# Performance work log

Hardware: AMD Instinct MI355X
Metric: run time of the kernel (lower is better)

## Reference

```python
import jax, jax.numpy as jnp
import numpy as np

N = 50000
E = 800000
IN_FT = 256
OUT_FT = 64


def setup_inputs() -> dict:
    key = jax.random.key(0)
    k_seq, k_w, k_src, k_dst, k_val = jax.random.split(key, 5)
    seq = jax.random.normal(k_seq, (N, IN_FT), dtype=jnp.float32)
    # xavier_uniform_ for fc.weight [out_ft, in_ft]
    limit = float(np.sqrt(6.0 / (IN_FT + OUT_FT)))
    W = jax.random.uniform(k_w, (OUT_FT, IN_FT), minval=-limit, maxval=limit, dtype=jnp.float32)
    bias = jnp.zeros((OUT_FT,), dtype=jnp.float32)          # bias.data.fill_(0.0)
    alpha = jnp.full((1,), 0.25, dtype=jnp.float32)         # PReLU default init
    edge_src = jax.random.randint(k_src, (E,), 0, N, dtype=jnp.int32)
    edge_dst = jax.random.randint(k_dst, (E,), 0, N, dtype=jnp.int32)
    edge_val = jax.random.uniform(k_val, (E,), dtype=jnp.float32)
    return {"seq": seq, "W": W, "bias": bias, "alpha": alpha,
            "edge_src": edge_src, "edge_dst": edge_dst, "edge_val": edge_val}


def reference(seq, W, bias, alpha, edge_src, edge_dst, edge_val):
    # fc(seq): [N, in_ft] @ [in_ft, out_ft] -> [N, out_ft]
    fts = jnp.einsum('ni,oi->no', seq, W)
    # spmm(adj, fts): gather source features, scale by edge value, scatter-add to dst
    msgs = fts[edge_src] * edge_val[:, None]                # [E, out_ft]
    out = jax.ops.segment_sum(msgs, edge_dst, num_segments=seq.shape[0])
    out = out + bias
    # PReLU with scalar (single-channel) alpha
    return jnp.where(out >= 0, out, alpha * out)
```

## Files before the change

### kernel.cpp

```cpp
#include <hip/hip_runtime.h>
#include <hip/hip_fp16.h>

#define IN_FT 256
#define OUT_FT 64

constexpr int BIN_LOG   = 6;
constexpr int BIN_NODES = 1 << BIN_LOG;
constexpr int MAX_NBIN  = 1024;
constexpr int BIN_CAP   = 1536;
constexpr int SC_BLOCKS = 256;

constexpr float FXS  = 2097152.0f;
constexpr float IFXS = 1.0f / 2097152.0f;

typedef _Float16 half8 __attribute__((ext_vector_type(8)));
typedef float    f32x4 __attribute__((ext_vector_type(4)));

__global__ __launch_bounds__(256) void wconv_kernel(
    const float* __restrict__ W, half8* __restrict__ Wh)
{
    int item = (int)blockIdx.x * 256 + (int)threadIdx.x;
    int l  = item & 63;
    int kc = (item >> 6) & 7;
    int nt = item >> 9;
    int m  = l & 15;
    int q  = l >> 4;
    const float* wp = W + (size_t)(nt * 16 + m) * IN_FT + kc * 32 + q * 8;
    float4 w0 = *(const float4*)wp;
    float4 w1 = *(const float4*)(wp + 4);
    half8 hh;
    hh[0] = (_Float16)w0.x; hh[1] = (_Float16)w0.y;
    hh[2] = (_Float16)w0.z; hh[3] = (_Float16)w0.w;
    hh[4] = (_Float16)w1.x; hh[5] = (_Float16)w1.y;
    hh[6] = (_Float16)w1.z; hh[7] = (_Float16)w1.w;
    Wh[item] = hh;
}

__global__ __launch_bounds__(256, 4) void fused_gemm_scatter(
    const float* __restrict__ seq, const half8* __restrict__ WhG,
    __half* __restrict__ fts, int N, int G,
    const int* __restrict__ src, const int* __restrict__ dst,
    const float* __restrict__ val, int* __restrict__ binCursor,
    int2* __restrict__ binned, int E, int NBIN)
{
    __shared__ alignas(16) char smem[32768];
    const int t = (int)threadIdx.x;

    if ((int)blockIdx.x < SC_BLOCKS) {
        int* h    = (int*)smem;
        int* base = h + MAX_NBIN;
        const int sb = (int)blockIdx.x;
        for (int i = t; i < NBIN; i += 256) h[i] = 0;
        __syncthreads();
        const int chunk = (E + SC_BLOCKS - 1) / SC_BLOCKS;
        const int s0 = sb * chunk;
        const int e0 = min(s0 + chunk, E);
#pragma unroll 4
        for (int i = s0 + t; i < e0; i += 256) atomicAdd(&h[dst[i] >> BIN_LOG], 1);
        __syncthreads();
        for (int i = t; i < NBIN; i += 256) {
            int c = h[i];
            base[i] = c ? atomicAdd(&binCursor[i], c) : 0;
            h[i] = 0;
        }
        __syncthreads();
#pragma unroll 4
        for (int i = s0 + t; i < e0; i += 256) {
            int d = dst[i];
            int b = d >> BIN_LOG;
            int pos = base[b] + atomicAdd(&h[b], 1);
            if (pos < BIN_CAP) {
                int2 pr;
                pr.x = src[i] | ((d & (BIN_NODES - 1)) << 16);
                pr.y = __float_as_int(val[i] * FXS);
                binned[(size_t)b * BIN_CAP + pos] = pr;
            }
        }
        return;
    }

    const int wave = t >> 6;
    const int l    = t & 63;
    int nodeBase = ((int)blockIdx.x - SC_BLOCKS) * 64 + wave * 16;
    const bool active = (nodeBase < N);
    if (nodeBase > N - 16) nodeBase = N - 16;
    const int m = l & 15;
    const int q = l >> 4;
    const float* ap = seq + (size_t)(nodeBase + m) * IN_FT + q * 8;

    float4 A[16];
#pragma unroll
    for (int kc = 0; kc < 8; ++kc) {
        A[2 * kc]     = *(const float4*)(ap + kc * 32);
        A[2 * kc + 1] = *(const float4*)(ap + kc * 32 + 4);
    }
    {
        const int4* wg  = (const int4*)WhG;
        int4*       bsw = (int4*)smem;
#pragma unroll
        for (int i = 0; i < 8; ++i) bsw[i * 256 + t] = wg[i * 256 + t];
    }
    __syncthreads();
    const half8* Bs = (const half8*)smem;

    f32x4 acc0 = {0.f, 0.f, 0.f, 0.f};
    f32x4 acc1 = {0.f, 0.f, 0.f, 0.f};
    f32x4 acc2 = {0.f, 0.f, 0.f, 0.f};
    f32x4 acc3 = {0.f, 0.f, 0.f, 0.f};

#pragma unroll
    for (int kc = 0; kc < 8; ++kc) {
        float4 c0 = A[2 * kc], c1 = A[2 * kc + 1];
        half8 af;
        af[0] = (_Float16)c0.x; af[1] = (_Float16)c0.y;
        af[2] = (_Float16)c0.z; af[3] = (_Float16)c0.w;
        af[4] = (_Float16)c1.x; af[5] = (_Float16)c1.y;
        af[6] = (_Float16)c1.z; af[7] = (_Float16)c1.w;

        half8 b0 = Bs[(0 * 8 + kc) * 64 + l];
        half8 b1 = Bs[(1 * 8 + kc) * 64 + l];
        half8 b2 = Bs[(2 * 8 + kc) * 64 + l];
        half8 b3 = Bs[(3 * 8 + kc) * 64 + l];
        acc0 = __builtin_amdgcn_mfma_f32_16x16x32_f16(af, b0, acc0, 0, 0, 0);
        acc1 = __builtin_amdgcn_mfma_f32_16x16x32_f16(af, b1, acc1, 0, 0, 0);
        acc2 = __builtin_amdgcn_mfma_f32_16x16x32_f16(af, b2, acc2, 0, 0, 0);
        acc3 = __builtin_amdgcn_mfma_f32_16x16x32_f16(af, b3, acc3, 0, 0, 0);
    }

    if (active) {
#pragma unroll
        for (int r = 0; r < 4; ++r) {
            int node = nodeBase + q * 4 + r;
            __half* op = fts + (size_t)node * OUT_FT + m;
            op[0]  = __float2half(acc0[r]);
            op[16] = __float2half(acc1[r]);
            op[32] = __float2half(acc2[r]);
            op[48] = __float2half(acc3[r]);
        }
    }
}

__global__ __launch_bounds__(512, 4) void bin_reduce(
    const int2* __restrict__ binned, const int* __restrict__ binCursor,
    const __half* __restrict__ fts, const float* __restrict__ bias,
    const float* __restrict__ alpha, float* __restrict__ out, int N)
{
    __shared__ int accum[BIN_NODES * OUT_FT];
    const int b    = (int)blockIdx.x;
    const int t    = (int)threadIdx.x;
    const int lane = t & 63;
    const int wv   = t >> 6;

    int4* a4 = (int4*)accum;
#pragma unroll
    for (int i = 0; i < (BIN_NODES * OUT_FT / 4) / 512; ++i)
        a4[i * 512 + t] = make_int4(0, 0, 0, 0);
    __syncthreads();

    const int nrec = min(binCursor[b], BIN_CAP);
    const int2* rec = binned + (size_t)b * BIN_CAP;
    const unsigned short* ftsu = (const unsigned short*)fts + lane;

    int i = wv * 16;
    for (; i + 16 <= nrec; i += 8 * 16) {
        int2 pr[16];
#pragma unroll
        for (int k = 0; k < 16; ++k) pr[k] = rec[i + k];
        __builtin_amdgcn_sched_barrier(0);
        unsigned short h[16];
#pragma unroll
        for (int k = 0; k < 16; ++k)
            h[k] = ftsu[(size_t)(pr[k].x & 0xFFFF) * OUT_FT];
        __builtin_amdgcn_sched_barrier(0);
#pragma unroll
        for (int k = 0; k < 16; ++k) {
            float p = __half2float(__ushort_as_half(h[k])) * __int_as_float(pr[k].y);
            atomicAdd(&accum[(pr[k].x >> 16) * OUT_FT + lane], __float2int_rn(p));
        }
    }
    for (; i < nrec; ++i) {
        int2 pr = rec[i];
        float fv = __half2float(__ushort_as_half(ftsu[(size_t)(pr.x & 0xFFFF) * OUT_FT]));
        atomicAdd(&accum[(pr.x >> 16) * OUT_FT + lane],
                  __float2int_rn(fv * __int_as_float(pr.y)));
    }
    __syncthreads();

    const float a = alpha[0];
    for (int j = t; j < BIN_NODES * (OUT_FT / 4); j += 512) {
        int row  = j >> 4;
        int c    = (j & 15) << 2;
        int node = (b << BIN_LOG) + row;
        if (node < N) {
            int4 v = *(int4*)&accum[row * OUT_FT + c];
            float4 o;
            float x0 = (float)v.x * IFXS + bias[c + 0];
            float x1 = (float)v.y * IFXS + bias[c + 1];
            float x2 = (float)v.z * IFXS + bias[c + 2];
            float x3 = (float)v.w * IFXS + bias[c + 3];
            o.x = (x0 >= 0.f) ? x0 : a * x0;
            o.y = (x1 >= 0.f) ? x1 : a * x1;
            o.z = (x2 >= 0.f) ? x2 : a * x2;
            o.w = (x3 >= 0.f) ? x3 : a * x3;
            *(float4*)(out + (size_t)node * OUT_FT + c) = o;
        }
    }
}

extern "C" void kernel_launch(void* const* d_in, const int* in_sizes, int n_in,
                              void* d_out, int out_size, void* d_ws, size_t ws_size,
                              hipStream_t stream) {
    const float* seq      = (const float*)d_in[0];
    const float* W        = (const float*)d_in[1];
    const float* bias     = (const float*)d_in[2];
    const float* alpha    = (const float*)d_in[3];
    const int*   edge_src = (const int*)d_in[4];
    const int*   edge_dst = (const int*)d_in[5];
    const float* edge_val = (const float*)d_in[6];
    float* out = (float*)d_out;

    const int N    = in_sizes[0] / IN_FT;
    const int E    = in_sizes[4];
    const int NBIN = (N + BIN_NODES - 1) >> BIN_LOG;

    size_t off = 0;
    auto take = [&](size_t bytes) -> char* {
        char* p = (char*)d_ws + off;
        off += (bytes + 255) & ~(size_t)255;
        return p;
    };
    __half* fts       = (__half*)take((size_t)N * OUT_FT * sizeof(__half));
    int*    binCursor = (int*)take((size_t)NBIN * sizeof(int));
    half8*  Wh        = (half8*)take((size_t)4 * 8 * 64 * sizeof(half8));
    int2*   binned    = (int2*)take((size_t)NBIN * BIN_CAP * sizeof(int2));
    (void)ws_size;

    hipMemsetAsync(binCursor, 0, (size_t)NBIN * sizeof(int), stream);

    wconv_kernel<<<8, 256, 0, stream>>>(W, Wh);

    const int G = (N + 63) / 64;
    fused_gemm_scatter<<<SC_BLOCKS + G, 256, 0, stream>>>(
        seq, Wh, fts, N, G, edge_src, edge_dst, edge_val,
        binCursor, binned, E, NBIN);

    bin_reduce<<<NBIN, 512, 0, stream>>>(
        binned, binCursor, fts, bias, alpha, out, N);
}
```

Baseline: 157.3 us.

## Replace global bin cursors with per-block segmented bins and prefix-sum compaction

The scatter phase now writes each edge record into a fixed per-(bin, scatter-block) segment, using only shared-memory atomics for the position. This removes the second pass over dst, the global atomicAdd on bin cursors and the memset. The reduce kernel loads the 256 per-segment counts, builds a compacted index list in LDS with a wave prefix scan, and then gathers records through that list. The costs are an extra indirection per record, a larger and sparser binned buffer, and a risk of silently dropping edges if any segment receives more than 20 records.

```diff
diff --git a/kernel.cpp b/kernel.cpp
--- a/kernel.cpp
+++ b/kernel.cpp
@@ -7,8 +7,9 @@
 constexpr int BIN_LOG   = 6;
 constexpr int BIN_NODES = 1 << BIN_LOG;
 constexpr int MAX_NBIN  = 1024;
-constexpr int BIN_CAP   = 1536;
 constexpr int SC_BLOCKS = 256;
+constexpr int SEG_CAP   = 20;
+constexpr int WORK_CAP  = 1536;
 
 constexpr float FXS  = 2097152.0f;
 constexpr float IFXS = 1.0f / 2097152.0f;
@@ -40,42 +41,57 @@
     const float* __restrict__ seq, const half8* __restrict__ WhG,
     __half* __restrict__ fts, int N, int G,
     const int* __restrict__ src, const int* __restrict__ dst,
-    const float* __restrict__ val, int* __restrict__ binCursor,
+    const float* __restrict__ val, int* __restrict__ cntG,
     int2* __restrict__ binned, int E, int NBIN)
 {
     __shared__ alignas(16) char smem[32768];
     const int t = (int)threadIdx.x;
 
     if ((int)blockIdx.x < SC_BLOCKS) {
-        int* h    = (int*)smem;
-        int* base = h + MAX_NBIN;
+        int* h = (int*)smem;
         const int sb = (int)blockIdx.x;
         for (int i = t; i < NBIN; i += 256) h[i] = 0;
         __syncthreads();
         const int chunk = (E + SC_BLOCKS - 1) / SC_BLOCKS;
         const int s0 = sb * chunk;
         const int e0 = min(s0 + chunk, E);
-#pragma unroll 4
-        for (int i = s0 + t; i < e0; i += 256) atomicAdd(&h[dst[i] >> BIN_LOG], 1);
-        __syncthreads();
-        for (int i = t; i < NBIN; i += 256) {
-            int c = h[i];
-            base[i] = c ? atomicAdd(&binCursor[i], c) : 0;
-            h[i] = 0;
-        }
-        __syncthreads();
-#pragma unroll 4
-        for (int i = s0 + t; i < e0; i += 256) {
+
+        int i = s0 + t;
+        for (; i + 768 < e0; i += 1024) {
+            int d[4], s[4]; float v[4];
+#pragma unroll
+            for (int k = 0; k < 4; ++k) {
+                d[k] = dst[i + k * 256];
+                s[k] = src[i + k * 256];
+                v[k] = val[i + k * 256];
+            }
+            __builtin_amdgcn_sched_barrier(0);
+#pragma unroll
+            for (int k = 0; k < 4; ++k) {
+                int b = d[k] >> BIN_LOG;
+                int pos = atomicAdd(&h[b], 1);
+                if (pos < SEG_CAP) {
+                    int2 pr;
+                    pr.x = s[k] | ((d[k] & (BIN_NODES - 1)) << 16);
+                    pr.y = __float_as_int(v[k] * FXS);
+                    binned[((size_t)b * SC_BLOCKS + sb) * SEG_CAP + pos] = pr;
+                }
+            }
+        }
+        for (; i < e0; i += 256) {
             int d = dst[i];
             int b = d >> BIN_LOG;
-            int pos = base[b] + atomicAdd(&h[b], 1);
-            if (pos < BIN_CAP) {
+            int pos = atomicAdd(&h[b], 1);
+            if (pos < SEG_CAP) {
                 int2 pr;
                 pr.x = src[i] | ((d & (BIN_NODES - 1)) << 16);
                 pr.y = __float_as_int(val[i] * FXS);
-                binned[(size_t)b * BIN_CAP + pos] = pr;
+                binned[((size_t)b * SC_BLOCKS + sb) * SEG_CAP + pos] = pr;
             }
         }
+        __syncthreads();
+        for (int b = t; b < NBIN; b += 256)
+            cntG[(size_t)b * SC_BLOCKS + sb] = h[b];
         return;
     }
 
@@ -141,11 +157,13 @@
 }
 
 __global__ __launch_bounds__(512, 4) void bin_reduce(
-    const int2* __restrict__ binned, const int* __restrict__ binCursor,
+    const int2* __restrict__ binned, const int* __restrict__ cntG,
     const __half* __restrict__ fts, const float* __restrict__ bias,
     const float* __restrict__ alpha, float* __restrict__ out, int N)
 {
     __shared__ int accum[BIN_NODES * OUT_FT];
+    __shared__ int work[WORK_CAP];
+    __shared__ int wsum[8];
     const int b    = (int)blockIdx.x;
     const int t    = (int)threadIdx.x;
     const int lane = t & 63;
@@ -155,17 +173,39 @@
 #pragma unroll
     for (int i = 0; i < (BIN_NODES * OUT_FT / 4) / 512; ++i)
         a4[i * 512 + t] = make_int4(0, 0, 0, 0);
-    __syncthreads();
-
-    const int nrec = min(binCursor[b], BIN_CAP);
-    const int2* rec = binned + (size_t)b * BIN_CAP;
+
+    int c = 0;
+    if (t < 256) c = min(cntG[(size_t)b * SC_BLOCKS + t], SEG_CAP);
+    int incl = c;
+#pragma unroll
+    for (int d = 1; d < 64; d <<= 1) {
+        int u = __shfl_up(incl, d, 64);
+        if (lane >= d) incl += u;
+    }
+    if (lane == 63) wsum[wv] = incl;
+    __syncthreads();
+    int woff = 0;
+#pragma unroll
+    for (int w = 0; w < 4; ++w) if (w < wv) woff += wsum[w];
+    const int tot = min(wsum[0] + wsum[1] + wsum[2] + wsum[3], WORK_CAP);
+    if (t < 256 && c > 0) {
+        int o    = woff + incl - c;
+        int base = t * SEG_CAP;
+        for (int j = 0; j < c && o + j < WORK_CAP; ++j) work[o + j] = base + j;
+    }
+    __syncthreads();
+
+    const int2* rec = binned + (size_t)b * SC_BLOCKS * SEG_CAP;
     const unsigned short* ftsu = (const unsigned short*)fts + lane;
 
     int i = wv * 16;
-    for (; i + 16 <= nrec; i += 8 * 16) {
+    for (; i + 16 <= tot; i += 8 * 16) {
+        int idx[16];
+#pragma unroll
+        for (int k = 0; k < 16; ++k) idx[k] = work[i + k];
         int2 pr[16];
 #pragma unroll
-        for (int k = 0; k < 16; ++k) pr[k] = rec[i + k];
+        for (int k = 0; k < 16; ++k) pr[k] = rec[idx[k]];
         __builtin_amdgcn_sched_barrier(0);
         unsigned short h[16];
 #pragma unroll
@@ -178,8 +218,8 @@
             atomicAdd(&accum[(pr[k].x >> 16) * OUT_FT + lane], __float2int_rn(p));
         }
     }
-    for (; i < nrec; ++i) {
-        int2 pr = rec[i];
+    for (; i < tot; ++i) {
+        int2 pr = rec[work[i]];
         float fv = __half2float(__ushort_as_half(ftsu[(size_t)(pr.x & 0xFFFF) * OUT_FT]));
         atomicAdd(&accum[(pr.x >> 16) * OUT_FT + lane],
                   __float2int_rn(fv * __int_as_float(pr.y)));
@@ -189,20 +229,20 @@
     const float a = alpha[0];
     for (int j = t; j < BIN_NODES * (OUT_FT / 4); j += 512) {
         int row  = j >> 4;
-        int c    = (j & 15) << 2;
+        int cc   = (j & 15) << 2;
         int node = (b << BIN_LOG) + row;
         if (node < N) {
-            int4 v = *(int4*)&accum[row * OUT_FT + c];
+            int4 v = *(int4*)&accum[row * OUT_FT + cc];
             float4 o;
-            float x0 = (float)v.x * IFXS + bias[c + 0];
-            float x1 = (float)v.y * IFXS + bias[c + 1];
-            float x2 = (float)v.z * IFXS + bias[c + 2];
-            float x3 = (float)v.w * IFXS + bias[c + 3];
+            float x0 = (float)v.x * IFXS + bias[cc + 0];
+            float x1 = (float)v.y * IFXS + bias[cc + 1];
+            float x2 = (float)v.z * IFXS + bias[cc + 2];
+            float x3 = (float)v.w * IFXS + bias[cc + 3];
             o.x = (x0 >= 0.f) ? x0 : a * x0;
             o.y = (x1 >= 0.f) ? x1 : a * x1;
             o.z = (x2 >= 0.f) ? x2 : a * x2;
             o.w = (x3 >= 0.f) ? x3 : a * x3;
-            *(float4*)(out + (size_t)node * OUT_FT + c) = o;
+            *(float4*)(out + (size_t)node * OUT_FT + cc) = o;
         }
     }
 }
@@ -229,21 +269,20 @@
         off += (bytes + 255) & ~(size_t)255;
         return p;
     };
-    __half* fts       = (__half*)take((size_t)N * OUT_FT * sizeof(__half));
-    int*    binCursor = (int*)take((size_t)NBIN * sizeof(int));
-    half8*  Wh        = (half8*)take((size_t)4 * 8 * 64 * sizeof(half8));
-    int2*   binned    = (int2*)take((size_t)NBIN * BIN_CAP * sizeof(int2));
+    __half* fts    = (__half*)take((size_t)N * OUT_FT * sizeof(__half));
+    int*    cntG   = (int*)take((size_t)NBIN * SC_BLOCKS * sizeof(int));
+    half8*  Wh     = (half8*)take((size_t)4 * 8 * 64 * sizeof(half8));
+    int2*   binned = (int2*)take((size_t)NBIN * SC_BLOCKS * SEG_CAP * sizeof(int2));
     (void)ws_size;
 
-    hipMemsetAsync(binCursor, 0, (size_t)NBIN * sizeof(int), stream);
 
     wconv_kernel<<<8, 256, 0, stream>>>(W, Wh);
 
     const int G = (N + 63) / 64;
     fused_gemm_scatter<<<SC_BLOCKS + G, 256, 0, stream>>>(
         seq, Wh, fts, N, G, edge_src, edge_dst, edge_val,
-        binCursor, binned, E, NBIN);
+        cntG, binned, E, NBIN);
 
     bin_reduce<<<NBIN, 512, 0, stream>>>(
-        binned, binCursor, fts, bias, alpha, out, N);
-}
+        binned, cntG, fts, bias, alpha, out, N);
+}
```

Result: slower. 170.1 us (+8.1%).
